# Optimization experiments

Hardware: AMD Instinct MI355X
Metric: run time of the kernel (lower is better)

The kernel has to match this reference:

```python
import jax, jax.numpy as jnp
import numpy as np

B, S, H = 2, 1024, 1024
E, I, K = 8, 3584, 2


def setup_inputs() -> dict:
    key = jax.random.key(0)
    k1, k2, k3, k4, k5 = jax.random.split(key, 5)
    scale_h = 1.0 / np.sqrt(H)
    scale_i = 1.0 / np.sqrt(I)
    return {
        "hidden_states": jax.random.normal(k1, (B, S, H), dtype=jnp.float32),
        "gate_w": jax.random.normal(k2, (E, H), dtype=jnp.float32) * scale_h,
        "w1": jax.random.normal(k3, (E, I, H), dtype=jnp.float32) * scale_h,
        "w2": jax.random.normal(k4, (E, H, I), dtype=jnp.float32) * scale_i,
        "w3": jax.random.normal(k5, (E, I, H), dtype=jnp.float32) * scale_h,
    }


def reference(hidden_states, gate_w, w1, w2, w3):
    b, s, h = hidden_states.shape
    x = hidden_states.reshape(-1, h)  # [T, H]
    # router: logits -> float32 softmax -> top-k -> renormalize
    router_logits = x @ gate_w.T  # [T, E]
    probs = jax.nn.softmax(router_logits.astype(jnp.float32), axis=-1)
    topw, topi = jax.lax.top_k(probs, K)  # [T, K]
    topw = topw / jnp.sum(topw, axis=-1, keepdims=True)
    topw = topw.astype(x.dtype)
    # per-token per-expert gate weight (0 for unselected experts) -> dense
    # combine is mathematically identical to gather/scatter dispatch
    gate = jnp.sum(jax.nn.one_hot(topi, E, dtype=x.dtype) * topw[..., None], axis=1)  # [T, E]
    # grouped SwiGLU FFN over all experts
    h1 = jnp.einsum('th,eih->tei', x, w1)
    h3 = jnp.einsum('th,eih->tei', x, w3)
    g = jax.nn.silu(h1) * h3  # [T, E, I]
    y = jnp.einsum('tei,ehi->teh', g, w2)  # [T, E, H]
    out = jnp.einsum('te,teh->th', gate, y)
    return out.reshape(b, s, h)
```

## Files before the change

kernel.cpp:

```cpp
#include <hip/hip_runtime.h>
#include <stdint.h>

#define T_TOK 2048
#define HDIM 1024
#define NEXP 8
#define IDIM 3584
#define MAXT1 24
#define MAXT2 40

#define WS_CNT   0
#define WS_BASE  64
#define WS_TE1   128
#define WS_TM1   224
#define WS_TE2   320
#define WS_TM2   480
#define WS_NT1   640
#define WS_NT2   644
#define WS_TOK   704
#define WS_GW    (WS_TOK + NEXP * T_TOK * 4)
#define WS_XB    (WS_GW + NEXP * T_TOK * 4)
#define WS_G     (WS_XB + T_TOK * HDIM * 2)

typedef __attribute__((ext_vector_type(8))) short bf16x8;
typedef __attribute__((ext_vector_type(16))) float f32x16;

__device__ __forceinline__ unsigned short f2bf(float f) {
    union { float f; unsigned int u; } a; a.f = f;
    unsigned int u = a.u;
    return (unsigned short)((u + 0x7fffu + ((u >> 16) & 1u)) >> 16);
}

__device__ __forceinline__ unsigned int cvt_pk_bf16(float lo, float hi) {
    unsigned int r;
    asm("v_cvt_pk_bf16_f32 %0, %1, %2" : "=v"(r) : "v"(lo), "v"(hi));
    return r;
}

__device__ __forceinline__ uint4 pack8(const float4 a, const float4 b) {
    uint4 r;
    r.x = cvt_pk_bf16(a.x, a.y);
    r.y = cvt_pk_bf16(a.z, a.w);
    r.z = cvt_pk_bf16(b.x, b.y);
    r.w = cvt_pk_bf16(b.z, b.w);
    return r;
}

__device__ __forceinline__ void gload16(const void* gsrc, void* ldst) {
    __builtin_amdgcn_global_load_lds(
        (const __attribute__((address_space(1))) unsigned int*)gsrc,
        (__attribute__((address_space(3))) unsigned int*)ldst, 16, 0, 0);
}

__global__ __launch_bounds__(256) void xcvt_kernel(
    const float* __restrict__ x, unsigned short* __restrict__ xb)
{
    int i = (blockIdx.x * 256 + threadIdx.x) * 8;
    float4 a = *(const float4*)(x + i);
    float4 b = *(const float4*)(x + i + 4);
    *(uint4*)(xb + i) = pack8(a, b);
}

__global__ __launch_bounds__(256) void router_kernel(
    const float* __restrict__ x, const float* __restrict__ gate_w,
    int* __restrict__ cnt, int* __restrict__ tok, float* __restrict__ gw)
{
    int t = blockIdx.x * 4 + (threadIdx.x >> 6);
    int lane = threadIdx.x & 63;
    if (t >= T_TOK) return;
    const float* xr = x + (size_t)t * HDIM;
    float part[NEXP];
#pragma unroll
    for (int e = 0; e < NEXP; e++) part[e] = 0.f;
    for (int h = lane; h < HDIM; h += 64) {
        float xv = xr[h];
#pragma unroll
        for (int e = 0; e < NEXP; e++) part[e] += xv * gate_w[e * HDIM + h];
    }
#pragma unroll
    for (int e = 0; e < NEXP; e++) {
        float v = part[e];
#pragma unroll
        for (int o = 32; o > 0; o >>= 1) v += __shfl_xor(v, o);
        part[e] = v;
    }
    if (lane == 0) {
        int i0 = 0; float v0 = part[0];
#pragma unroll
        for (int e = 1; e < NEXP; e++) if (part[e] > v0) { v0 = part[e]; i0 = e; }
        int i1 = -1; float v1 = -3.4e38f;
#pragma unroll
        for (int e = 0; e < NEXP; e++) if (e != i0 && part[e] > v1) { v1 = part[e]; i1 = e; }
        float d = __expf(v1 - v0);
        float w1v = d / (1.f + d);
        float w0v = 1.f - w1v;
        int p0 = atomicAdd(&cnt[i0], 1);
        tok[i0 * T_TOK + p0] = t; gw[i0 * T_TOK + p0] = w0v;
        int p1 = atomicAdd(&cnt[i1], 1);
        tok[i1 * T_TOK + p1] = t; gw[i1 * T_TOK + p1] = w1v;
    }
}

__global__ void scan_kernel(const int* __restrict__ cnt, int* __restrict__ base,
                            int* __restrict__ tE1, int* __restrict__ tM1,
                            int* __restrict__ nt1p,
                            int* __restrict__ tE2, int* __restrict__ tM2,
                            int* __restrict__ nt2p)
{
    if (threadIdx.x == 0) {
        int s = 0, n1 = 0, n2 = 0;
        for (int e = 0; e < NEXP; e++) {
            base[e] = s; s += cnt[e];
            for (int m0 = 0; m0 < cnt[e]; m0 += 256) { tE1[n1] = e; tM1[n1] = m0; n1++; }
            for (int m0 = 0; m0 < cnt[e]; m0 += 128) { tE2[n2] = e; tM2[n2] = m0; n2++; }
        }
        *nt1p = n1; *nt2p = n2;
    }
}

__global__ __launch_bounds__(256, 2) void ffn1_mfma(
    const unsigned short* __restrict__ xb,
    const float* __restrict__ w1,
    const float* __restrict__ w3,
    const int* __restrict__ cnt, const int* __restrict__ base,
    const int* __restrict__ tok,
    const int* __restrict__ tileE, const int* __restrict__ tileM,
    const int* __restrict__ ntot,
    unsigned short* __restrict__ g)
{
    const int ti = blockIdx.y;
    if (ti >= *ntot) return;
    const int e = tileE[ti];
    const int m0 = tileM[ti];
    const int cntE = cnt[e];
    const int i0 = blockIdx.x * 64;
    const int tid = threadIdx.x;
    const int lane = tid & 63;
    const int wid = tid >> 6;

    __shared__ __align__(16) unsigned char lds[40960];

    const unsigned short* xsrc[4];
    {
        int row = wid * 64 + lane;
        int t = tok[e * T_TOK + min(m0 + row, cntE - 1)];
#pragma unroll
        for (int q = 0; q < 4; q++)
            xsrc[q] = xb + (size_t)t * HDIM + q * 8;
    }
    const unsigned xldst = (unsigned)(wid * 1024);

    const int srow = tid >> 2;
    const int kq = tid & 3;
    const unsigned wdst = (unsigned)(kq * 1024 + srow * 16);
    const float* w1e = w1 + ((size_t)e * IDIM + i0 + srow) * HDIM + kq * 8;
    const float* w3e = w3 + ((size_t)e * IDIM + i0 + srow) * HDIM + kq * 8;

    f32x16 acc1[2][2], acc3[2][2];
#pragma unroll
    for (int a = 0; a < 2; a++)
#pragma unroll
        for (int b = 0; b < 2; b++)
#pragma unroll
            for (int r = 0; r < 16; r++) { acc1[a][b][r] = 0.f; acc3[a][b][r] = 0.f; }

    const int fr = lane & 31;
    const int hi = lane >> 5;

    float4 wva[2], wvb[2];

#pragma unroll
    for (int q = 0; q < 4; q++)
        gload16(xsrc[q], lds + (unsigned)(q * 4096) + xldst);
    wva[0] = *(const float4*)(w1e);  wva[1] = *(const float4*)(w1e + 4);
    wvb[0] = *(const float4*)(w3e);  wvb[1] = *(const float4*)(w3e + 4);

    const int NST = HDIM / 32;
#pragma unroll 1
    for (int st = 0; st < NST; st++) {
        const unsigned xsb = (unsigned)(st & 1) * 16384u;
        __syncthreads();
        *(uint4*)(lds + 32768u + wdst) = pack8(wva[0], wva[1]);
        *(uint4*)(lds + 36864u + wdst) = pack8(wvb[0], wvb[1]);
        __syncthreads();

        if (st + 1 < NST) {
            const int kn = (st + 1) * 32;
            const unsigned xnb = xsb ^ 16384u;
#pragma unroll
            for (int q = 0; q < 4; q++)
                gload16(xsrc[q] + kn, lds + xnb + (unsigned)(q * 4096) + xldst);
            wva[0] = *(const float4*)(w1e + kn);  wva[1] = *(const float4*)(w1e + kn + 4);
            wvb[0] = *(const float4*)(w3e + kn);  wvb[1] = *(const float4*)(w3e + kn + 4);
        }

#pragma unroll
        for (int c = 0; c < 2; c++) {
            const unsigned ch = (unsigned)((c * 2 + hi) * 4096);
            const unsigned chw = (unsigned)((c * 2 + hi) * 1024);
            bf16x8 a0 = *(const bf16x8*)(lds + xsb + ch + (wid * 64 + fr) * 16);
            bf16x8 a1 = *(const bf16x8*)(lds + xsb + ch + (wid * 64 + 32 + fr) * 16);
            bf16x8 p0 = *(const bf16x8*)(lds + 32768u + chw + fr * 16);
            bf16x8 p1 = *(const bf16x8*)(lds + 32768u + chw + (32 + fr) * 16);
            bf16x8 q0 = *(const bf16x8*)(lds + 36864u + chw + fr * 16);
            bf16x8 q1 = *(const bf16x8*)(lds + 36864u + chw + (32 + fr) * 16);
            acc1[0][0] = __builtin_amdgcn_mfma_f32_32x32x16_bf16(a0, p0, acc1[0][0], 0, 0, 0);
            acc1[0][1] = __builtin_amdgcn_mfma_f32_32x32x16_bf16(a0, p1, acc1[0][1], 0, 0, 0);
            acc1[1][0] = __builtin_amdgcn_mfma_f32_32x32x16_bf16(a1, p0, acc1[1][0], 0, 0, 0);
            acc1[1][1] = __builtin_amdgcn_mfma_f32_32x32x16_bf16(a1, p1, acc1[1][1], 0, 0, 0);
            acc3[0][0] = __builtin_amdgcn_mfma_f32_32x32x16_bf16(a0, q0, acc3[0][0], 0, 0, 0);
            acc3[0][1] = __builtin_amdgcn_mfma_f32_32x32x16_bf16(a0, q1, acc3[0][1], 0, 0, 0);
            acc3[1][0] = __builtin_amdgcn_mfma_f32_32x32x16_bf16(a1, q0, acc3[1][0], 0, 0, 0);
            acc3[1][1] = __builtin_amdgcn_mfma_f32_32x32x16_bf16(a1, q1, acc3[1][1], 0, 0, 0);
        }
    }

    const int pbase = base[e] + m0;
    const int rb4 = 4 * hi;
#pragma unroll
    for (int m = 0; m < 2; m++) {
#pragma unroll
        for (int r = 0; r < 16; r++) {
            int row = (r & 3) + 8 * (r >> 2) + rb4;
            int mm = wid * 64 + m * 32 + row;
            if (m0 + mm < cntE) {
                unsigned short* grow = g + (size_t)(pbase + mm) * IDIM + i0 + fr;
#pragma unroll
                for (int n = 0; n < 2; n++) {
                    float h1 = acc1[m][n][r], h3 = acc3[m][n][r];
                    float v = (h1 / (1.f + __expf(-h1))) * h3;
                    grow[n * 32] = f2bf(v);
                }
            }
        }
    }
}

__global__ __launch_bounds__(256, 4) void ffn2_mfma(
    const unsigned short* __restrict__ g,
    const float* __restrict__ w2,
    const int* __restrict__ cnt, const int* __restrict__ base,
    const int* __restrict__ tok, const float* __restrict__ gw,
    const int* __restrict__ tileE, const int* __restrict__ tileM,
    const int* __restrict__ ntot,
    float* __restrict__ out)
{
    const int ti = blockIdx.y;
    if (ti >= *ntot) return;
    const int e = tileE[ti];
    const int m0 = tileM[ti];
    const int cntE = cnt[e];
    const int pane = blockIdx.x;
    const int h0 = (pane & 15) * 64;
    const int ks = pane >> 4;
    const int tid = threadIdx.x;
    const int lane = tid & 63;
    const int wid = tid >> 6;

    __shared__ __align__(16) unsigned char lds[40960];

    const int kbeg = ks * (IDIM / 4);

    const int xrr = (lane >> 3);
    const unsigned xoff = ((((unsigned)(lane & 7)) * 16) ^ (((unsigned)xrr) << 4)) >> 1;
    const unsigned short* gsrc[4];
    const int be = base[e];
#pragma unroll
    for (int i = 0; i < 4; i++) {
        int row = wid * 32 + i * 8 + xrr;
        int grow = be + min(m0 + row, cntE - 1);
        gsrc[i] = g + (size_t)grow * IDIM + kbeg + xoff;
    }

    const int rw = tid >> 2;
    const int kq = tid & 3;
    const unsigned swzW = ((unsigned)(rw & 7)) << 4;
    const unsigned wd0 = (((unsigned)kq) * 32) ^ swzW;
    const unsigned wd1 = (((unsigned)kq) * 32 + 16) ^ swzW;
    const float* w2e = w2 + ((size_t)e * HDIM + h0 + rw) * IDIM + kbeg + kq * 16;

    f32x16 acc[2];
#pragma unroll
    for (int a = 0; a < 2; a++)
#pragma unroll
        for (int r = 0; r < 16; r++) acc[a][r] = 0.f;

    const int wr = wid >> 1;
    const int wc = wid & 1;
    const unsigned lrow = (unsigned)(lane & 31);
    const unsigned lswz = (lrow & 7) << 4;
    const unsigned hi16 = (unsigned)((lane >> 5) * 16);
    const unsigned aRow = (wr * 64 + lrow) * 128;
    const unsigned bRow = 32768u + (wc * 32 + lrow) * 128;

    float4 wv[4];
#pragma unroll
    for (int i = 0; i < 4; i++)
        gload16(gsrc[i], lds + (wid * 32 + i * 8) * 128);
#pragma unroll
    for (int i = 0; i < 4; i++)
        wv[i] = *(const float4*)(w2e + i * 4);

    const int NST = (IDIM / 4) / 64;
    for (int st = 0; st < NST; st++) {
        const unsigned xsb = (unsigned)(st & 1) * 16384u;
        const int k0 = st * 64;
        __syncthreads();
        *(uint4*)(lds + 32768u + rw * 128 + wd0) = pack8(wv[0], wv[1]);
        *(uint4*)(lds + 32768u + rw * 128 + wd1) = pack8(wv[2], wv[3]);
        __syncthreads();

        if (st + 1 < NST) {
            const unsigned xnb = xsb ^ 16384u;
#pragma unroll
            for (int i = 0; i < 4; i++)
                gload16(gsrc[i] + k0 + 64, lds + xnb + (wid * 32 + i * 8) * 128);
#pragma unroll
            for (int i = 0; i < 4; i++)
                wv[i] = *(const float4*)(w2e + k0 + 64 + i * 4);
        }

#pragma unroll
        for (int s = 0; s < 4; s++) {
            const unsigned off = (((unsigned)(s * 32)) + hi16) ^ lswz;
            bf16x8 a0 = *(const bf16x8*)(lds + xsb + aRow + off);
            bf16x8 a1 = *(const bf16x8*)(lds + xsb + aRow + 32 * 128 + off);
            bf16x8 b0 = *(const bf16x8*)(lds + bRow + off);
            acc[0] = __builtin_amdgcn_mfma_f32_32x32x16_bf16(a0, b0, acc[0], 0, 0, 0);
            acc[1] = __builtin_amdgcn_mfma_f32_32x32x16_bf16(a1, b0, acc[1], 0, 0, 0);
        }
    }

    const int rb4 = 4 * (lane >> 5);
    const int hcol = h0 + wc * 32 + (int)lrow;
#pragma unroll
    for (int ma = 0; ma < 2; ma++) {
#pragma unroll
        for (int r = 0; r < 16; r++) {
            int row = (r & 3) + 8 * (r >> 2) + rb4;
            int m = wr * 64 + ma * 32 + row;
            if (m0 + m < cntE) {
                int idx = e * T_TOK + m0 + m;
                int t = tok[idx];
                float wgt = gw[idx];
                atomicAdd(out + (size_t)t * HDIM + hcol, wgt * acc[ma][r]);
            }
        }
    }
}

extern "C" void kernel_launch(void* const* d_in, const int* in_sizes, int n_in,
                              void* d_out, int out_size, void* d_ws, size_t ws_size,
                              hipStream_t stream) {
    const float* x      = (const float*)d_in[0];
    const float* gate_w = (const float*)d_in[1];
    const float* w1     = (const float*)d_in[2];
    const float* w2     = (const float*)d_in[3];
    const float* w3     = (const float*)d_in[4];
    float* out = (float*)d_out;
    char* ws = (char*)d_ws;
    int* cnt   = (int*)(ws + WS_CNT);
    int* base  = (int*)(ws + WS_BASE);
    int* tE1   = (int*)(ws + WS_TE1);
    int* tM1   = (int*)(ws + WS_TM1);
    int* tE2   = (int*)(ws + WS_TE2);
    int* tM2   = (int*)(ws + WS_TM2);
    int* nt1   = (int*)(ws + WS_NT1);
    int* nt2   = (int*)(ws + WS_NT2);
    int* tok   = (int*)(ws + WS_TOK);
    float* gw  = (float*)(ws + WS_GW);
    unsigned short* xb = (unsigned short*)(ws + WS_XB);
    unsigned short* g  = (unsigned short*)(ws + WS_G);

    hipMemsetAsync(cnt, 0, 64, stream);
    hipMemsetAsync(d_out, 0, (size_t)out_size * sizeof(float), stream);

    xcvt_kernel<<<T_TOK * HDIM / (256 * 8), 256, 0, stream>>>(x, xb);
    router_kernel<<<T_TOK / 4, 256, 0, stream>>>(x, gate_w, cnt, tok, gw);
    scan_kernel<<<1, 64, 0, stream>>>(cnt, base, tE1, tM1, nt1, tE2, tM2, nt2);
    ffn1_mfma<<<dim3(IDIM / 64, MAXT1), 256, 0, stream>>>(xb, w1, w3, cnt, base, tok, tE1, tM1, nt1, g);
    ffn2_mfma<<<dim3(64, MAXT2), 256, 0, stream>>>(g, w2, cnt, base, tok, gw, tE2, tM2, nt2, out);
}
```

Baseline: 379.7 us.

## Swizzle ffn1 LDS layout and widen ffn2 tiles to 128 columns

```diff
diff --git a/kernel.cpp b/kernel.cpp
--- a/kernel.cpp
+++ b/kernel.cpp
@@ -117,7 +117,7 @@
     }
 }
 
-__global__ __launch_bounds__(256, 2) void ffn1_mfma(
+__global__ __launch_bounds__(256, 3) void ffn1_mfma(
     const unsigned short* __restrict__ xb,
     const float* __restrict__ w1,
     const float* __restrict__ w3,
@@ -139,21 +139,22 @@
 
     __shared__ __align__(16) unsigned char lds[40960];
 
+    const int xrr = (lane >> 2);
+    const unsigned xoff = ((((unsigned)(lane & 3)) * 16) ^ (((unsigned)(xrr & 3)) << 4)) >> 1;
     const unsigned short* xsrc[4];
-    {
-        int row = wid * 64 + lane;
+#pragma unroll
+    for (int i = 0; i < 4; i++) {
+        int row = wid * 64 + i * 16 + xrr;
         int t = tok[e * T_TOK + min(m0 + row, cntE - 1)];
-#pragma unroll
-        for (int q = 0; q < 4; q++)
-            xsrc[q] = xb + (size_t)t * HDIM + q * 8;
-    }
-    const unsigned xldst = (unsigned)(wid * 1024);
-
-    const int srow = tid >> 2;
+        xsrc[i] = xb + (size_t)t * HDIM + xoff;
+    }
+    const unsigned xdst = (unsigned)(wid * 4096);
+
+    const int rw = tid >> 2;
     const int kq = tid & 3;
-    const unsigned wdst = (unsigned)(kq * 1024 + srow * 16);
-    const float* w1e = w1 + ((size_t)e * IDIM + i0 + srow) * HDIM + kq * 8;
-    const float* w3e = w3 + ((size_t)e * IDIM + i0 + srow) * HDIM + kq * 8;
+    const unsigned wd = (((unsigned)kq) * 16) ^ (((unsigned)(rw & 3)) << 4);
+    const float* w1e = w1 + ((size_t)e * IDIM + i0 + rw) * HDIM + kq * 8;
+    const float* w3e = w3 + ((size_t)e * IDIM + i0 + rw) * HDIM + kq * 8;
 
     f32x16 acc1[2][2], acc3[2][2];
 #pragma unroll
@@ -165,44 +166,52 @@
 
     const int fr = lane & 31;
     const int hi = lane >> 5;
+    const unsigned lswz = ((unsigned)(fr & 3)) << 4;
+    const unsigned hi16 = (unsigned)(hi * 16);
+    const unsigned aBase = (unsigned)((wid * 64 + fr) * 64);
+    const unsigned bBase = (unsigned)(fr * 64);
 
     float4 wva[2], wvb[2];
 
 #pragma unroll
-    for (int q = 0; q < 4; q++)
-        gload16(xsrc[q], lds + (unsigned)(q * 4096) + xldst);
-    wva[0] = *(const float4*)(w1e);  wva[1] = *(const float4*)(w1e + 4);
-    wvb[0] = *(const float4*)(w3e);  wvb[1] = *(const float4*)(w3e + 4);
+    for (int i = 0; i < 4; i++)
+        gload16(xsrc[i], lds + xdst + (unsigned)(i * 1024));
+    wva[0] = *(const float4*)(w1e);
+    wva[1] = *(const float4*)(w1e + 4);
+    wvb[0] = *(const float4*)(w3e);
+    wvb[1] = *(const float4*)(w3e + 4);
 
     const int NST = HDIM / 32;
 #pragma unroll 1
     for (int st = 0; st < NST; st++) {
         const unsigned xsb = (unsigned)(st & 1) * 16384u;
+        const int k0 = st * 32;
         __syncthreads();
-        *(uint4*)(lds + 32768u + wdst) = pack8(wva[0], wva[1]);
-        *(uint4*)(lds + 36864u + wdst) = pack8(wvb[0], wvb[1]);
+        *(uint4*)(lds + 32768u + rw * 64 + wd) = pack8(wva[0], wva[1]);
+        *(uint4*)(lds + 36864u + rw * 64 + wd) = pack8(wvb[0], wvb[1]);
         __syncthreads();
 
-        if (st + 1 < NST) {
-            const int kn = (st + 1) * 32;
+        if (k0 + 32 < HDIM) {
+            const int kn = k0 + 32;
             const unsigned xnb = xsb ^ 16384u;
 #pragma unroll
-            for (int q = 0; q < 4; q++)
-                gload16(xsrc[q] + kn, lds + xnb + (unsigned)(q * 4096) + xldst);
-            wva[0] = *(const float4*)(w1e + kn);  wva[1] = *(const float4*)(w1e + kn + 4);
-            wvb[0] = *(const float4*)(w3e + kn);  wvb[1] = *(const float4*)(w3e + kn + 4);
-        }
-
-#pragma unroll
-        for (int c = 0; c < 2; c++) {
-            const unsigned ch = (unsigned)((c * 2 + hi) * 4096);
-            const unsigned chw = (unsigned)((c * 2 + hi) * 1024);
-            bf16x8 a0 = *(const bf16x8*)(lds + xsb + ch + (wid * 64 + fr) * 16);
-            bf16x8 a1 = *(const bf16x8*)(lds + xsb + ch + (wid * 64 + 32 + fr) * 16);
-            bf16x8 p0 = *(const bf16x8*)(lds + 32768u + chw + fr * 16);
-            bf16x8 p1 = *(const bf16x8*)(lds + 32768u + chw + (32 + fr) * 16);
-            bf16x8 q0 = *(const bf16x8*)(lds + 36864u + chw + fr * 16);
-            bf16x8 q1 = *(const bf16x8*)(lds + 36864u + chw + (32 + fr) * 16);
+            for (int i = 0; i < 4; i++)
+                gload16(xsrc[i] + kn, lds + xnb + xdst + (unsigned)(i * 1024));
+            wva[0] = *(const float4*)(w1e + kn);
+            wva[1] = *(const float4*)(w1e + kn + 4);
+            wvb[0] = *(const float4*)(w3e + kn);
+            wvb[1] = *(const float4*)(w3e + kn + 4);
+        }
+
+#pragma unroll
+        for (int s = 0; s < 2; s++) {
+            const unsigned off = (((unsigned)(s * 32)) + hi16) ^ lswz;
+            bf16x8 a0 = *(const bf16x8*)(lds + xsb + aBase + off);
+            bf16x8 a1 = *(const bf16x8*)(lds + xsb + aBase + 32 * 64 + off);
+            bf16x8 p0 = *(const bf16x8*)(lds + 32768u + bBase + off);
+            bf16x8 p1 = *(const bf16x8*)(lds + 32768u + bBase + 32 * 64 + off);
+            bf16x8 q0 = *(const bf16x8*)(lds + 36864u + bBase + off);
+            bf16x8 q1 = *(const bf16x8*)(lds + 36864u + bBase + 32 * 64 + off);
             acc1[0][0] = __builtin_amdgcn_mfma_f32_32x32x16_bf16(a0, p0, acc1[0][0], 0, 0, 0);
             acc1[0][1] = __builtin_amdgcn_mfma_f32_32x32x16_bf16(a0, p1, acc1[0][1], 0, 0, 0);
             acc1[1][0] = __builtin_amdgcn_mfma_f32_32x32x16_bf16(a1, p0, acc1[1][0], 0, 0, 0);
@@ -235,7 +244,7 @@
     }
 }
 
-__global__ __launch_bounds__(256, 4) void ffn2_mfma(
+__global__ __launch_bounds__(256, 3) void ffn2_mfma(
     const unsigned short* __restrict__ g,
     const float* __restrict__ w2,
     const int* __restrict__ cnt, const int* __restrict__ base,
@@ -250,13 +259,13 @@
     const int m0 = tileM[ti];
     const int cntE = cnt[e];
     const int pane = blockIdx.x;
-    const int h0 = (pane & 15) * 64;
-    const int ks = pane >> 4;
+    const int h0 = (pane & 7) * 128;
+    const int ks = pane >> 3;
     const int tid = threadIdx.x;
     const int lane = tid & 63;
     const int wid = tid >> 6;
 
-    __shared__ __align__(16) unsigned char lds[40960];
+    __shared__ __align__(16) unsigned char lds[49152];
 
     const int kbeg = ks * (IDIM / 4);
 
@@ -277,61 +286,77 @@
     const unsigned wd0 = (((unsigned)kq) * 32) ^ swzW;
     const unsigned wd1 = (((unsigned)kq) * 32 + 16) ^ swzW;
     const float* w2e = w2 + ((size_t)e * HDIM + h0 + rw) * IDIM + kbeg + kq * 16;
-
-    f32x16 acc[2];
+    const size_t rhalf = (size_t)64 * IDIM;
+
+    f32x16 acc[2][2];
 #pragma unroll
     for (int a = 0; a < 2; a++)
 #pragma unroll
-        for (int r = 0; r < 16; r++) acc[a][r] = 0.f;
+        for (int b = 0; b < 2; b++)
+#pragma unroll
+            for (int r = 0; r < 16; r++) acc[a][b][r] = 0.f;
 
     const int wr = wid >> 1;
     const int wc = wid & 1;
     const unsigned lrow = (unsigned)(lane & 31);
     const unsigned lswz = (lrow & 7) << 4;
     const unsigned hi16 = (unsigned)((lane >> 5) * 16);
-    const unsigned aRow = (wr * 64 + lrow) * 128;
-    const unsigned bRow = 32768u + (wc * 32 + lrow) * 128;
-
-    float4 wv[4];
+    const unsigned aOff = (wr * 64 + lrow) * 128;
+    const unsigned bOff = 32768u + (wc * 64 + lrow) * 128;
+    const unsigned xdst = (unsigned)(wid * 32) * 128;
+
+    float4 wv[2][4];
+
 #pragma unroll
     for (int i = 0; i < 4; i++)
-        gload16(gsrc[i], lds + (wid * 32 + i * 8) * 128);
-#pragma unroll
-    for (int i = 0; i < 4; i++)
-        wv[i] = *(const float4*)(w2e + i * 4);
+        gload16(gsrc[i], lds + xdst + (unsigned)(i * 8) * 128);
+#pragma unroll
+    for (int h = 0; h < 2; h++)
+#pragma unroll
+        for (int i = 0; i < 4; i++)
+            wv[h][i] = *(const float4*)(w2e + h * rhalf + i * 4);
 
     const int NST = (IDIM / 4) / 64;
     for (int st = 0; st < NST; st++) {
         const unsigned xsb = (unsigned)(st & 1) * 16384u;
         const int k0 = st * 64;
         __syncthreads();
-        *(uint4*)(lds + 32768u + rw * 128 + wd0) = pack8(wv[0], wv[1]);
-        *(uint4*)(lds + 32768u + rw * 128 + wd1) = pack8(wv[2], wv[3]);
+#pragma unroll
+        for (int h = 0; h < 2; h++) {
+            *(uint4*)(lds + 32768u + (rw + h * 64) * 128 + wd0) = pack8(wv[h][0], wv[h][1]);
+            *(uint4*)(lds + 32768u + (rw + h * 64) * 128 + wd1) = pack8(wv[h][2], wv[h][3]);
+        }
         __syncthreads();
 
         if (st + 1 < NST) {
+            const int kn = k0 + 64;
             const unsigned xnb = xsb ^ 16384u;
 #pragma unroll
             for (int i = 0; i < 4; i++)
-                gload16(gsrc[i] + k0 + 64, lds + xnb + (wid * 32 + i * 8) * 128);
-#pragma unroll
-            for (int i = 0; i < 4; i++)
-                wv[i] = *(const float4*)(w2e + k0 + 64 + i * 4);
+                gload16(gsrc[i] + kn, lds + xnb + xdst + (unsigned)(i * 8) * 128);
+#pragma unroll
+            for (int h = 0; h < 2; h++)
+#pragma unroll
+                for (int i = 0; i < 4; i++)
+                    wv[h][i] = *(const float4*)(w2e + h * rhalf + kn + i * 4);
         }
 
 #pragma unroll
         for (int s = 0; s < 4; s++) {
             const unsigned off = (((unsigned)(s * 32)) + hi16) ^ lswz;
-            bf16x8 a0 = *(const bf16x8*)(lds + xsb + aRow + off);
-            bf16x8 a1 = *(const bf16x8*)(lds + xsb + aRow + 32 * 128 + off);
-            bf16x8 b0 = *(const bf16x8*)(lds + bRow + off);
-            acc[0] = __builtin_amdgcn_mfma_f32_32x32x16_bf16(a0, b0, acc[0], 0, 0, 0);
-            acc[1] = __builtin_amdgcn_mfma_f32_32x32x16_bf16(a1, b0, acc[1], 0, 0, 0);
+            bf16x8 a0 = *(const bf16x8*)(lds + xsb + aOff + off);
+            bf16x8 a1 = *(const bf16x8*)(lds + xsb + aOff + 32 * 128 + off);
+            bf16x8 b0 = *(const bf16x8*)(lds + bOff + off);
+            bf16x8 b1 = *(const bf16x8*)(lds + bOff + 32 * 128 + off);
+            acc[0][0] = __builtin_amdgcn_mfma_f32_32x32x16_bf16(a0, b0, acc[0][0], 0, 0, 0);
+            acc[0][1] = __builtin_amdgcn_mfma_f32_32x32x16_bf16(a0, b1, acc[0][1], 0, 0, 0);
+            acc[1][0] = __builtin_amdgcn_mfma_f32_32x32x16_bf16(a1, b0, acc[1][0], 0, 0, 0);
+            acc[1][1] = __builtin_amdgcn_mfma_f32_32x32x16_bf16(a1, b1, acc[1][1], 0, 0, 0);
         }
     }
 
     const int rb4 = 4 * (lane >> 5);
-    const int hcol = h0 + wc * 32 + (int)lrow;
+    const int hcol = h0 + wc * 64 + (int)lrow;
 #pragma unroll
     for (int ma = 0; ma < 2; ma++) {
 #pragma unroll
@@ -342,7 +367,8 @@
                 int idx = e * T_TOK + m0 + m;
                 int t = tok[idx];
                 float wgt = gw[idx];
-                atomicAdd(out + (size_t)t * HDIM + hcol, wgt * acc[ma][r]);
+                atomicAdd(out + (size_t)t * HDIM + hcol,      wgt * acc[ma][0][r]);
+                atomicAdd(out + (size_t)t * HDIM + hcol + 32, wgt * acc[ma][1][r]);
             }
         }
     }
@@ -378,5 +404,5 @@
     router_kernel<<<T_TOK / 4, 256, 0, stream>>>(x, gate_w, cnt, tok, gw);
     scan_kernel<<<1, 64, 0, stream>>>(cnt, base, tE1, tM1, nt1, tE2, tM2, nt2);
     ffn1_mfma<<<dim3(IDIM / 64, MAXT1), 256, 0, stream>>>(xb, w1, w3, cnt, base, tok, tE1, tM1, nt1, g);
-    ffn2_mfma<<<dim3(64, MAXT2), 256, 0, stream>>>(g, w2, cnt, base, tok, gw, tE2, tM2, nt2, out);
-}
+    ffn2_mfma<<<dim3(32, MAXT2), 256, 0, stream>>>(g, w2, cnt, base, tok, gw, tE2, tM2, nt2, out);
+}
```

Result: slower. 429.4 us (+13.1%).
